# Kernel tuning notes

Hardware: AMD Instinct MI355X
Metric: run time of the kernel (lower is better)

## Reference

```python
import jax, jax.numpy as jnp
import numpy as np


def setup_inputs() -> dict:
    key = jax.random.key(0)
    k1, k2 = jax.random.split(key)
    B, N, D, T = 32, 1024, 512, 4096
    x = jax.random.normal(k1, (B, N, D), dtype=jnp.float32)
    durations = jax.random.randint(k2, (B, N), 0, 8, dtype=jnp.int64)
    return {"x": x, "durations": durations, "target_len": T}


def reference(x, durations, target_len):
    """Vectorized length regulator.

    For each output frame t, the source phoneme index is
    searchsorted(cumsum(durations), t, side='right'): frame t belongs to
    phoneme i iff csum[i-1] <= t < csum[i]. This replaces the per-batch
    repeat_interleave loop with a single gather.
    """
    B, N, D = x.shape
    T = target_len
    dur = durations.astype(jnp.int32)
    csum = jnp.cumsum(dur, axis=1)           # (B, N)
    total = csum[:, -1]                       # (B,) valid frames per batch
    t = jnp.arange(T, dtype=jnp.int32)        # (T,)
    # per-batch frame -> phoneme index
    idx = jax.vmap(lambda c: jnp.searchsorted(c, t, side='right'))(csum)  # (B, T)
    mask = t[None, :] < total[:, None]        # (B, T)
    idx_c = jnp.clip(idx, 0, N - 1)
    gathered = jnp.take_along_axis(x, idx_c[:, :, None], axis=1)  # (B, T, D)
    expanded = jnp.where(mask[:, :, None], gathered, jnp.zeros((), x.dtype))
    return expanded, mask
```

## Files before the change

kernel.cpp:

```cpp
#include <hip/hip_runtime.h>

#define B_ 32
#define N_ 1024
#define D_ 512
#define T_ 4096
#define D4_ (D_ / 4)

__global__ __launch_bounds__(N_) void lr_scan_kernel(
    const int* __restrict__ dur,
    int* __restrict__ idxmap,
    float* __restrict__ mask_out)
{
    __shared__ int s[N_];
    const int b = blockIdx.x;
    const int tid = threadIdx.x;

    s[tid] = dur[b * N_ + tid];
    __syncthreads();

    for (int off = 1; off < N_; off <<= 1) {
        int add = (tid >= off) ? s[tid - off] : 0;
        __syncthreads();
        s[tid] += add;
        __syncthreads();
    }

    const int end   = s[tid];
    const int start = (tid == 0) ? 0 : s[tid - 1];
    const int total = s[N_ - 1];

    const int cs = min(start, T_);
    const int ce = min(end,   T_);
    for (int t = cs; t < ce; ++t) {
        idxmap[b * T_ + t] = tid;
    }

    for (int t = total + tid; t < T_; t += N_) {
        idxmap[b * T_ + t] = -1;
    }

    for (int t = tid; t < T_; t += N_) {
        mask_out[b * T_ + t] = (t < total) ? 1.0f : 0.0f;
    }
}

__global__ __launch_bounds__(256) void lr_gather_kernel(
    const float4* __restrict__ x,
    const int* __restrict__ idxmap,
    float4* __restrict__ out)
{
    const int total4 = B_ * T_ * D4_;
    const int stride = gridDim.x * blockDim.x;
    for (int gid = blockIdx.x * blockDim.x + threadIdx.x;
         gid < total4; gid += stride) {
        const int frame = gid >> 7;
        const int d4    = gid & (D4_ - 1);
        const int idx   = idxmap[frame];
        float4 val;
        if (idx >= 0) {
            const int b = frame >> 12;
            val = x[(b * N_ + idx) * D4_ + d4];
        } else {
            val = make_float4(0.f, 0.f, 0.f, 0.f);
        }
        out[gid] = val;
    }
}

extern "C" void kernel_launch(void* const* d_in, const int* in_sizes, int n_in,
                              void* d_out, int out_size, void* d_ws, size_t ws_size,
                              hipStream_t stream) {
    const float* x   = (const float*)d_in[0];
    const int*   dur = (const int*)d_in[1];

    float* out      = (float*)d_out;
    float* mask_out = out + (size_t)B_ * T_ * D_;
    int*   idxmap   = (int*)d_ws;

    lr_scan_kernel<<<B_, N_, 0, stream>>>(dur, idxmap, mask_out);
    lr_gather_kernel<<<2048, 256, 0, stream>>>((const float4*)x, idxmap,
                                               (float4*)out);
}
```

Measured before the change: 319.1 us.

## Use wave-shuffle scan and batched nontemporal gather with 8 loads per thread

The shared-memory Hillis-Steele scan becomes a two-level wavefront shuffle scan, which removes most of the barriers. The gather kernel now launches one block per 2048 float4 elements and has each thread load 8 indices and 8 rows before storing any of them. This raises memory-level parallelism. Each index is made wave-uniform with readfirstlane, which relies on all 64 lanes of a wave falling in the same frame. Output is written with nontemporal stores so the 256 MB result does not pollute the cache.

```diff
diff --git a/kernel.cpp b/kernel.cpp
--- a/kernel.cpp
+++ b/kernel.cpp
@@ -6,28 +6,44 @@
 #define T_ 4096
 #define D4_ (D_ / 4)
 
+typedef float f4_t __attribute__((ext_vector_type(4)));
+
 __global__ __launch_bounds__(N_) void lr_scan_kernel(
     const int* __restrict__ dur,
     int* __restrict__ idxmap,
     float* __restrict__ mask_out)
 {
-    __shared__ int s[N_];
+    __shared__ int wsum[16];
     const int b = blockIdx.x;
     const int tid = threadIdx.x;
+    const int lane = tid & 63;
+    const int wave = tid >> 6;
 
-    s[tid] = dur[b * N_ + tid];
+    const int d = dur[b * N_ + tid];
+
+    int v = d;
+#pragma unroll
+    for (int off = 1; off < 64; off <<= 1) {
+        int u = __shfl_up(v, off, 64);
+        if (lane >= off) v += u;
+    }
+    if (lane == 63) wsum[wave] = v;
     __syncthreads();
 
-    for (int off = 1; off < N_; off <<= 1) {
-        int add = (tid >= off) ? s[tid - off] : 0;
-        __syncthreads();
-        s[tid] += add;
-        __syncthreads();
+    if (tid < 16) {
+        int w = wsum[tid];
+#pragma unroll
+        for (int off = 1; off < 16; off <<= 1) {
+            int u = __shfl_up(w, off, 16);
+            if (tid >= off) w += u;
+        }
+        wsum[tid] = w;
     }
+    __syncthreads();
 
-    const int end   = s[tid];
-    const int start = (tid == 0) ? 0 : s[tid - 1];
-    const int total = s[N_ - 1];
+    const int end   = v + (wave ? wsum[wave - 1] : 0);
+    const int start = end - d;
+    const int total = wsum[15];
 
     const int cs = min(start, T_);
     const int ce = min(end,   T_);
@@ -45,25 +61,34 @@
 }
 
 __global__ __launch_bounds__(256) void lr_gather_kernel(
-    const float4* __restrict__ x,
+    const f4_t* __restrict__ x,
     const int* __restrict__ idxmap,
-    float4* __restrict__ out)
+    f4_t* __restrict__ out)
 {
-    const int total4 = B_ * T_ * D4_;
-    const int stride = gridDim.x * blockDim.x;
-    for (int gid = blockIdx.x * blockDim.x + threadIdx.x;
-         gid < total4; gid += stride) {
-        const int frame = gid >> 7;
-        const int d4    = gid & (D4_ - 1);
-        const int idx   = idxmap[frame];
-        float4 val;
+    const int base = blockIdx.x * 2048 + threadIdx.x;
+
+    int idxs[8];
+#pragma unroll
+    for (int k = 0; k < 8; ++k) {
+        idxs[k] = idxmap[(base + k * 256) >> 7];
+    }
+
+    f4_t vals[8];
+#pragma unroll
+    for (int k = 0; k < 8; ++k) {
+        const int gid = base + k * 256;
+        const int idx = __builtin_amdgcn_readfirstlane(idxs[k]);
         if (idx >= 0) {
-            const int b = frame >> 12;
-            val = x[(b * N_ + idx) * D4_ + d4];
+            const int b = gid >> 19;
+            vals[k] = x[(b * N_ + idx) * D4_ + (gid & (D4_ - 1))];
         } else {
-            val = make_float4(0.f, 0.f, 0.f, 0.f);
+            vals[k] = (f4_t){0.f, 0.f, 0.f, 0.f};
         }
-        out[gid] = val;
+    }
+
+#pragma unroll
+    for (int k = 0; k < 8; ++k) {
+        __builtin_nontemporal_store(vals[k], &out[base + k * 256]);
     }
 }
 
@@ -78,6 +103,8 @@
     int*   idxmap   = (int*)d_ws;
 
     lr_scan_kernel<<<B_, N_, 0, stream>>>(dur, idxmap, mask_out);
-    lr_gather_kernel<<<2048, 256, 0, stream>>>((const float4*)x, idxmap,
-                                               (float4*)out);
+
+    const int total4 = B_ * T_ * D4_;
+    lr_gather_kernel<<<total4 / 2048, 256, 0, stream>>>(
+        (const f4_t*)x, idxmap, (f4_t*)out);
 }
```

After: 368.1 us. +15.3%, slower.
